# Optimization experiments

Measured on AMD Instinct MI355X. Metric: run time of the kernel, lower is better.

The kernel has to match this reference:

```python
import jax, jax.numpy as jnp
import numpy as np

A = 312          # nb_attributes
LAT = 64         # latent_dim per attribute
HID = 128        # hidden_dim per attribute
OUT = 1          # output_dim per attribute
B = 8192         # batch


def setup_inputs() -> dict:
    key = jax.random.key(0)
    k1, k2, k3, k4, k5 = jax.random.split(key, 5)
    x = jax.random.normal(k1, (B, A * LAT), dtype=jnp.float32)
    # block-diagonal weights: one small matrix per attribute
    W1 = jax.random.normal(k2, (A, LAT, HID), dtype=jnp.float32) * (1.0 / np.sqrt(LAT))
    b1 = jax.random.normal(k3, (A, HID), dtype=jnp.float32) * 0.01
    W2 = jax.random.normal(k4, (A, HID, OUT), dtype=jnp.float32) * (1.0 / np.sqrt(HID))
    b2 = jax.random.normal(k5, (A, OUT), dtype=jnp.float32) * 0.01
    return {"x": x, "W1": W1, "b1": b1, "W2": W2, "b2": b2}


def reference(x, W1, b1, W2, b2):
    # BlockLinear 1: [B, A*LAT] -> view [B, A, LAT] -> per-attribute matmul -> [B, A, HID]
    xb = x.reshape(B, A, LAT)
    h = jnp.einsum('bal,alh->bah', xb, W1) + b1[None]   # [B, A, HID]
    h = jax.nn.relu(h)
    # BlockLinear 2: [B, A, HID] -> [B, A, OUT]
    o = jnp.einsum('bah,aho->bao', h, W2) + b2[None]    # [B, A, OUT]
    o = jax.nn.sigmoid(o)
    return o.reshape(B, A * OUT)
```

## Files before the change

### kernel.cpp

```cpp
#include <hip/hip_runtime.h>
#include <hip/hip_bf16.h>

#define NA   312
#define LAT  64
#define HID  128
#define NB   8192
#define MB   256
#define NBT  (NB / MB)
#define MT   4

typedef __attribute__((ext_vector_type(8))) short bf16x8;
typedef __attribute__((ext_vector_type(4))) float f32x4;

__device__ inline short f2bf(float f) {
    unsigned u = __builtin_bit_cast(unsigned, f);
    u += 0x7FFFu + ((u >> 16) & 1u);
    return (short)(u >> 16);
}

__device__ inline bf16x8 pack8(float4 v0, float4 v1) {
    __hip_bfloat162 c[4] = {
        __float22bfloat162_rn(float2{v0.x, v0.y}),
        __float22bfloat162_rn(float2{v0.z, v0.w}),
        __float22bfloat162_rn(float2{v1.x, v1.y}),
        __float22bfloat162_rn(float2{v1.z, v1.w})};
    bf16x8 f;
    __builtin_memcpy(&f, &c[0], 16);
    return f;
}

__global__ __launch_bounds__(256, 2) void prep_w1(
    const float* __restrict__ W1, short* __restrict__ w1f)
{
    __shared__ float lds[LAT * HID];
    const int a   = blockIdx.x;
    const int tid = threadIdx.x;

    const float4* src = reinterpret_cast<const float4*>(W1 + (size_t)a * (LAT * HID));
    float4* ldsv = reinterpret_cast<float4*>(lds);
    #pragma unroll
    for (int i = 0; i < (LAT * HID / 4) / 256; ++i)
        ldsv[i * 256 + tid] = src[i * 256 + tid];
    __syncthreads();

    bf16x8* dst = reinterpret_cast<bf16x8*>(w1f + (size_t)a * (LAT * HID));
    #pragma unroll
    for (int i = 0; i < 4; ++i) {
        const int e    = i * 256 + tid;
        const int nt   = e >> 7;
        const int kk   = (e >> 6) & 1;
        const int lane = e & 63;
        const int n  = nt * 16 + (lane & 15);
        const int k0 = kk * 32 + (lane >> 4) * 8;
        bf16x8 f;
        #pragma unroll
        for (int j = 0; j < 8; ++j)
            f[j] = f2bf(lds[(k0 + j) * HID + n]);
        dst[e] = f;
    }
}

__global__ __launch_bounds__(256, 2) void attr_decoder_main(
    const float* __restrict__ x,
    const short* __restrict__ w1f,
    const float* __restrict__ b1,
    const float* __restrict__ W2,
    const float* __restrict__ b2,
    float* __restrict__ out)
{
    const int tid  = threadIdx.x;
    const int a    = blockIdx.x >> 5;
    const int bt   = blockIdx.x & (NBT - 1);
    const int w    = tid >> 6;
    const int lane = tid & 63;
    const int llo  = lane & 15;
    const int lhi  = lane >> 4;
    const int rowbase = bt * MB + w * 64;

    bf16x8 afrag[MT][2];
    #pragma unroll
    for (int mt = 0; mt < MT; ++mt) {
        const float* xrow = x + (size_t)(rowbase + mt * 16 + llo) * (NA * LAT)
                              + (size_t)a * LAT;
        #pragma unroll
        for (int kk = 0; kk < 2; ++kk) {
            const float4* p = reinterpret_cast<const float4*>(xrow + kk * 32 + lhi * 8);
            afrag[mt][kk] = pack8(p[0], p[1]);
        }
    }

    const bf16x8* wf = reinterpret_cast<const bf16x8*>(w1f + (size_t)a * (LAT * HID));
    const float*  b1a = b1 + a * HID;
    const float*  w2a = W2 + a * HID;
    float p2[MT][4] = {};
    #pragma unroll 4
    for (int nt = 0; nt < 8; ++nt) {
        const bf16x8 bf0 = wf[(nt * 2 + 0) * 64 + lane];
        const bf16x8 bf1 = wf[(nt * 2 + 1) * 64 + lane];
        const int n = nt * 16 + llo;
        const float b1v = b1a[n];
        const float w2v = w2a[n];
        const f32x4 cin = {b1v, b1v, b1v, b1v};
        #pragma unroll
        for (int mt = 0; mt < MT; ++mt) {
            f32x4 acc = cin;
            acc = __builtin_amdgcn_mfma_f32_16x16x32_bf16(afrag[mt][0], bf0, acc, 0, 0, 0);
            acc = __builtin_amdgcn_mfma_f32_16x16x32_bf16(afrag[mt][1], bf1, acc, 0, 0, 0);
            #pragma unroll
            for (int r = 0; r < 4; ++r)
                p2[mt][r] = fmaf(fmaxf(acc[r], 0.f), w2v, p2[mt][r]);
        }
    }

    const float ob = b2[a];
    #pragma unroll
    for (int mt = 0; mt < MT; ++mt) {
        #pragma unroll
        for (int r = 0; r < 4; ++r) {
            float s = p2[mt][r];
            s += __shfl_xor(s, 1);
            s += __shfl_xor(s, 2);
            s += __shfl_xor(s, 4);
            s += __shfl_xor(s, 8);
            s = 1.0f / (1.0f + __expf(-(s + ob)));
            if (llo == 0) {
                const int row = rowbase + mt * 16 + lhi * 4 + r;
                out[(size_t)row * NA + a] = s;
            }
        }
    }
}

extern "C" void kernel_launch(void* const* d_in, const int* in_sizes, int n_in,
                              void* d_out, int out_size, void* d_ws, size_t ws_size,
                              hipStream_t stream) {
    const float* x  = (const float*)d_in[0];
    const float* W1 = (const float*)d_in[1];
    const float* b1 = (const float*)d_in[2];
    const float* W2 = (const float*)d_in[3];
    const float* b2 = (const float*)d_in[4];
    float* out = (float*)d_out;
    short* w1f = (short*)d_ws;

    hipLaunchKernelGGL(prep_w1, dim3(NA), dim3(256), 0, stream, W1, w1f);
    hipLaunchKernelGGL(attr_decoder_main, dim3(NA * NBT), dim3(256), 0, stream,
                       x, w1f, b1, W2, b2, out);
}
```

Before: 179.3 us.

## Convert main kernel to persistent grid with register double-buffered x prefetch

The main kernel now launches a fixed grid of 512 blocks that loop over tiles, and each tile is processed in two 32-row halves. The raw fp32 x loads for the next half or next tile are issued into registers before the current half's MFMA work, so memory latency overlaps compute. Tile order also changes so consecutive blocks take different attributes of the same batch tile. The cost is fewer resident blocks for latency hiding, extra live registers for the prefetch buffer, and more loop and index overhead per tile.

```diff
diff --git a/kernel.cpp b/kernel.cpp
--- a/kernel.cpp
+++ b/kernel.cpp
@@ -7,7 +7,8 @@
 #define NB   8192
 #define MB   256
 #define NBT  (NB / MB)
-#define MT   4
+#define NT   (NA * NBT)
+#define GRID 512
 
 typedef __attribute__((ext_vector_type(8))) short bf16x8;
 typedef __attribute__((ext_vector_type(4))) float f32x4;
@@ -60,6 +61,25 @@
     }
 }
 
+#define ISSUE_LOADS(T, H)                                                       \
+    do {                                                                        \
+        const int a_  = (T) % NA;                                               \
+        const int bt_ = (T) / NA;                                               \
+        const int rb_ = bt_ * MB + w * 64 + (H) * 32;                           \
+        _Pragma("unroll")                                                       \
+        for (int mt = 0; mt < 2; ++mt) {                                        \
+            const float* xrow_ = x + (size_t)(rb_ + mt * 16 + llo) * (NA * LAT) \
+                                   + (size_t)a_ * LAT;                          \
+            _Pragma("unroll")                                                   \
+            for (int kk = 0; kk < 2; ++kk) {                                    \
+                const float4* p_ = reinterpret_cast<const float4*>(             \
+                    xrow_ + kk * 32 + lhi * 8);                                 \
+                xr[mt * 4 + kk * 2 + 0] = p_[0];                                \
+                xr[mt * 4 + kk * 2 + 1] = p_[1];                                \
+            }                                                                   \
+        }                                                                       \
+    } while (0)
+
 __global__ __launch_bounds__(256, 2) void attr_decoder_main(
     const float* __restrict__ x,
     const short* __restrict__ w1f,
@@ -69,65 +89,80 @@
     float* __restrict__ out)
 {
     const int tid  = threadIdx.x;
-    const int a    = blockIdx.x >> 5;
-    const int bt   = blockIdx.x & (NBT - 1);
     const int w    = tid >> 6;
     const int lane = tid & 63;
     const int llo  = lane & 15;
     const int lhi  = lane >> 4;
-    const int rowbase = bt * MB + w * 64;
 
-    bf16x8 afrag[MT][2];
-    #pragma unroll
-    for (int mt = 0; mt < MT; ++mt) {
-        const float* xrow = x + (size_t)(rowbase + mt * 16 + llo) * (NA * LAT)
-                              + (size_t)a * LAT;
-        #pragma unroll
-        for (int kk = 0; kk < 2; ++kk) {
-            const float4* p = reinterpret_cast<const float4*>(xrow + kk * 32 + lhi * 8);
-            afrag[mt][kk] = pack8(p[0], p[1]);
-        }
-    }
+    float4 xr[8];
 
-    const bf16x8* wf = reinterpret_cast<const bf16x8*>(w1f + (size_t)a * (LAT * HID));
-    const float*  b1a = b1 + a * HID;
-    const float*  w2a = W2 + a * HID;
-    float p2[MT][4] = {};
-    #pragma unroll 4
-    for (int nt = 0; nt < 8; ++nt) {
-        const bf16x8 bf0 = wf[(nt * 2 + 0) * 64 + lane];
-        const bf16x8 bf1 = wf[(nt * 2 + 1) * 64 + lane];
-        const int n = nt * 16 + llo;
-        const float b1v = b1a[n];
-        const float w2v = w2a[n];
-        const f32x4 cin = {b1v, b1v, b1v, b1v};
-        #pragma unroll
-        for (int mt = 0; mt < MT; ++mt) {
-            f32x4 acc = cin;
-            acc = __builtin_amdgcn_mfma_f32_16x16x32_bf16(afrag[mt][0], bf0, acc, 0, 0, 0);
-            acc = __builtin_amdgcn_mfma_f32_16x16x32_bf16(afrag[mt][1], bf1, acc, 0, 0, 0);
+    int t = blockIdx.x;
+    if (t >= NT) return;
+    ISSUE_LOADS(t, 0);
+
+    while (true) {
+        #pragma unroll 1
+        for (int h = 0; h < 2; ++h) {
+            bf16x8 af[2][2];
             #pragma unroll
-            for (int r = 0; r < 4; ++r)
-                p2[mt][r] = fmaf(fmaxf(acc[r], 0.f), w2v, p2[mt][r]);
-        }
-    }
+            for (int mt = 0; mt < 2; ++mt)
+                #pragma unroll
+                for (int kk = 0; kk < 2; ++kk)
+                    af[mt][kk] = pack8(xr[mt * 4 + kk * 2], xr[mt * 4 + kk * 2 + 1]);
 
-    const float ob = b2[a];
-    #pragma unroll
-    for (int mt = 0; mt < MT; ++mt) {
-        #pragma unroll
-        for (int r = 0; r < 4; ++r) {
-            float s = p2[mt][r];
-            s += __shfl_xor(s, 1);
-            s += __shfl_xor(s, 2);
-            s += __shfl_xor(s, 4);
-            s += __shfl_xor(s, 8);
-            s = 1.0f / (1.0f + __expf(-(s + ob)));
-            if (llo == 0) {
-                const int row = rowbase + mt * 16 + lhi * 4 + r;
-                out[(size_t)row * NA + a] = s;
+            const int tn = (h == 0) ? t : t + GRID;
+            if (h == 0) {
+                ISSUE_LOADS(tn, 1);
+            } else if (tn < NT) {
+                ISSUE_LOADS(tn, 0);
+            }
+
+            const int a  = t % NA;
+            const int bt = t / NA;
+            const bf16x8* wf  = reinterpret_cast<const bf16x8*>(w1f + (size_t)a * (LAT * HID));
+            const float*  b1a = b1 + a * HID;
+            const float*  w2a = W2 + a * HID;
+            float p2[2][4] = {};
+            #pragma unroll 4
+            for (int nt = 0; nt < 8; ++nt) {
+                const bf16x8 bf0 = wf[(nt * 2 + 0) * 64 + lane];
+                const bf16x8 bf1 = wf[(nt * 2 + 1) * 64 + lane];
+                const int n = nt * 16 + llo;
+                const float b1v = b1a[n];
+                const float w2v = w2a[n];
+                const f32x4 cin = {b1v, b1v, b1v, b1v};
+                #pragma unroll
+                for (int mt = 0; mt < 2; ++mt) {
+                    f32x4 acc = cin;
+                    acc = __builtin_amdgcn_mfma_f32_16x16x32_bf16(af[mt][0], bf0, acc, 0, 0, 0);
+                    acc = __builtin_amdgcn_mfma_f32_16x16x32_bf16(af[mt][1], bf1, acc, 0, 0, 0);
+                    #pragma unroll
+                    for (int r = 0; r < 4; ++r)
+                        p2[mt][r] = fmaf(fmaxf(acc[r], 0.f), w2v, p2[mt][r]);
+                }
+            }
+
+            const float ob = b2[a];
+            const int rowbase = bt * MB + w * 64 + h * 32;
+            #pragma unroll
+            for (int mt = 0; mt < 2; ++mt) {
+                #pragma unroll
+                for (int r = 0; r < 4; ++r) {
+                    float s = p2[mt][r];
+                    s += __shfl_xor(s, 1);
+                    s += __shfl_xor(s, 2);
+                    s += __shfl_xor(s, 4);
+                    s += __shfl_xor(s, 8);
+                    s = 1.0f / (1.0f + __expf(-(s + ob)));
+                    if (llo == 0) {
+                        const int row = rowbase + mt * 16 + lhi * 4 + r;
+                        out[(size_t)row * NA + a] = s;
+                    }
+                }
             }
         }
+        t += GRID;
+        if (t >= NT) break;
     }
 }
 
@@ -143,6 +178,6 @@
     short* w1f = (short*)d_ws;
 
     hipLaunchKernelGGL(prep_w1, dim3(NA), dim3(256), 0, stream, W1, w1f);
-    hipLaunchKernelGGL(attr_decoder_main, dim3(NA * NBT), dim3(256), 0, stream,
+    hipLaunchKernelGGL(attr_decoder_main, dim3(GRID), dim3(256), 0, stream,
                        x, w1f, b1, W2, b2, out);
 }
```

New measurement: 268.1 us. 1.5x slower.

## Stage contiguous x tiles for eight attributes in swizzled LDS per block

Applied to the files above, without the earlier changes.

Each block now covers 8 attributes by 64 rows instead of one attribute by 256 rows. It loads a contiguous 2KB row slice of x, converts it to bf16 and stores it in LDS with an XOR swizzle. Per-attribute A fragments are then read from LDS. The goal is coalesced global reads of x, which was previously fetched in 256-byte strided chunks per row, and a grid of 4992 blocks. In exchange, W1 fragments are reloaded per 16-row wave instead of being reused across 4 m-tiles, the attribute loop is serialized with less MFMA ILP, and LDS is added.

```diff
diff --git a/kernel.cpp b/kernel.cpp
--- a/kernel.cpp
+++ b/kernel.cpp
@@ -5,9 +5,10 @@
 #define LAT  64
 #define HID  128
 #define NB   8192
-#define MB   256
-#define NBT  (NB / MB)
-#define MT   4
+#define AG   8
+#define NAG  (NA / AG)
+#define RB   64
+#define NBT  (NB / RB)
 
 typedef __attribute__((ext_vector_type(8))) short bf16x8;
 typedef __attribute__((ext_vector_type(4))) float f32x4;
@@ -68,63 +69,70 @@
     const float* __restrict__ b2,
     float* __restrict__ out)
 {
+    __shared__ short xs[RB * AG * LAT];
+
     const int tid  = threadIdx.x;
-    const int a    = blockIdx.x >> 5;
+    const int ag   = blockIdx.x >> 7;
     const int bt   = blockIdx.x & (NBT - 1);
+    const int row0 = bt * RB;
+
+    {
+        const int lt = tid & 63;
+        const int rw = tid >> 6;
+        bf16x8* xs16 = reinterpret_cast<bf16x8*>(xs);
+        #pragma unroll
+        for (int i = 0; i < 16; ++i) {
+            const int r = i * 4 + rw;
+            const float4* p = reinterpret_cast<const float4*>(
+                x + (size_t)(row0 + r) * (NA * LAT) + ag * (AG * LAT)) + lt * 2;
+            xs16[r * 64 + (lt ^ (r & 7))] = pack8(p[0], p[1]);
+        }
+    }
+    __syncthreads();
+
     const int w    = tid >> 6;
     const int lane = tid & 63;
     const int llo  = lane & 15;
     const int lhi  = lane >> 4;
-    const int rowbase = bt * MB + w * 64;
+    const int arow = w * 16 + llo;
+    const bf16x8* xsv = reinterpret_cast<const bf16x8*>(xs);
 
-    bf16x8 afrag[MT][2];
-    #pragma unroll
-    for (int mt = 0; mt < MT; ++mt) {
-        const float* xrow = x + (size_t)(rowbase + mt * 16 + llo) * (NA * LAT)
-                              + (size_t)a * LAT;
+    #pragma unroll 1
+    for (int al = 0; al < AG; ++al) {
+        const int a = ag * AG + al;
+        const bf16x8 af0 = xsv[arow * 64 + ((al * 8 +     lhi) ^ (arow & 7))];
+        const bf16x8 af1 = xsv[arow * 64 + ((al * 8 + 4 + lhi) ^ (arow & 7))];
+
+        const bf16x8* wf  = reinterpret_cast<const bf16x8*>(w1f + (size_t)a * (LAT * HID));
+        const float*  b1a = b1 + a * HID;
+        const float*  w2a = W2 + a * HID;
+        float p2[4] = {};
         #pragma unroll
-        for (int kk = 0; kk < 2; ++kk) {
-            const float4* p = reinterpret_cast<const float4*>(xrow + kk * 32 + lhi * 8);
-            afrag[mt][kk] = pack8(p[0], p[1]);
-        }
-    }
-
-    const bf16x8* wf = reinterpret_cast<const bf16x8*>(w1f + (size_t)a * (LAT * HID));
-    const float*  b1a = b1 + a * HID;
-    const float*  w2a = W2 + a * HID;
-    float p2[MT][4] = {};
-    #pragma unroll 4
-    for (int nt = 0; nt < 8; ++nt) {
-        const bf16x8 bf0 = wf[(nt * 2 + 0) * 64 + lane];
-        const bf16x8 bf1 = wf[(nt * 2 + 1) * 64 + lane];
-        const int n = nt * 16 + llo;
-        const float b1v = b1a[n];
-        const float w2v = w2a[n];
-        const f32x4 cin = {b1v, b1v, b1v, b1v};
-        #pragma unroll
-        for (int mt = 0; mt < MT; ++mt) {
-            f32x4 acc = cin;
-            acc = __builtin_amdgcn_mfma_f32_16x16x32_bf16(afrag[mt][0], bf0, acc, 0, 0, 0);
-            acc = __builtin_amdgcn_mfma_f32_16x16x32_bf16(afrag[mt][1], bf1, acc, 0, 0, 0);
+        for (int nt = 0; nt < 8; ++nt) {
+            const bf16x8 bf0 = wf[(nt * 2 + 0) * 64 + lane];
+            const bf16x8 bf1 = wf[(nt * 2 + 1) * 64 + lane];
+            const int n = nt * 16 + llo;
+            const float b1v = b1a[n];
+            const float w2v = w2a[n];
+            f32x4 acc = {b1v, b1v, b1v, b1v};
+            acc = __builtin_amdgcn_mfma_f32_16x16x32_bf16(af0, bf0, acc, 0, 0, 0);
+            acc = __builtin_amdgcn_mfma_f32_16x16x32_bf16(af1, bf1, acc, 0, 0, 0);
             #pragma unroll
             for (int r = 0; r < 4; ++r)
-                p2[mt][r] = fmaf(fmaxf(acc[r], 0.f), w2v, p2[mt][r]);
+                p2[r] = fmaf(fmaxf(acc[r], 0.f), w2v, p2[r]);
         }
-    }
 
-    const float ob = b2[a];
-    #pragma unroll
-    for (int mt = 0; mt < MT; ++mt) {
+        const float ob = b2[a];
         #pragma unroll
         for (int r = 0; r < 4; ++r) {
-            float s = p2[mt][r];
+            float s = p2[r];
             s += __shfl_xor(s, 1);
             s += __shfl_xor(s, 2);
             s += __shfl_xor(s, 4);
             s += __shfl_xor(s, 8);
             s = 1.0f / (1.0f + __expf(-(s + ob)));
             if (llo == 0) {
-                const int row = rowbase + mt * 16 + lhi * 4 + r;
+                const int row = row0 + w * 16 + lhi * 4 + r;
                 out[(size_t)row * NA + a] = s;
             }
         }
@@ -143,6 +151,6 @@
     short* w1f = (short*)d_ws;
 
     hipLaunchKernelGGL(prep_w1, dim3(NA), dim3(256), 0, stream, W1, w1f);
-    hipLaunchKernelGGL(attr_decoder_main, dim3(NA * NBT), dim3(256), 0, stream,
+    hipLaunchKernelGGL(attr_decoder_main, dim3(NAG * NBT), dim3(256), 0, stream,
                        x, w1f, b1, W2, b2, out);
 }
```

New measurement: 249.3 us. 1.39x slower.
